# Kernel optimization log

Hardware: AMD Instinct MI355X
Metric: run time of the kernel (lower is better)

## Reference

```python
import jax, jax.numpy as jnp
import numpy as np

C = 128   # desc_dim
NQ = 8
NK = 32768

def setup_inputs() -> dict:
    k = jax.random.key(0)
    ks = jax.random.split(k, 9)
    query = jax.random.normal(ks[0], (1, C, NQ), dtype=jnp.float32)
    keys = jax.random.normal(ks[1], (1, C, NK), dtype=jnp.float32)
    value = jax.random.normal(ks[2], (1, C, NK), dtype=jnp.float32)
    dist = jax.random.normal(ks[3], (1, C, NQ * NK), dtype=jnp.float32)
    mask = jax.random.randint(ks[4], (1, NQ, NK), 0, 2).astype(bool)
    # MLP([3C, C, 1]) as 1x1 Conv1d weights (kernel size 1 -> plain matmuls)
    W1 = jax.random.normal(ks[5], (C, 3 * C), dtype=jnp.float32) * (1.0 / np.sqrt(3 * C))
    b1 = jax.random.normal(ks[6], (C,), dtype=jnp.float32) * 0.01
    W2 = jax.random.normal(ks[7], (1, C), dtype=jnp.float32) * (1.0 / np.sqrt(C))
    b2 = jax.random.normal(ks[8], (1,), dtype=jnp.float32) * 0.01
    return {"query": query, "keys": keys, "value": value, "dist": dist,
            "mask": mask, "W1": W1, "b1": b1, "W2": W2, "b2": b2}

def reference(query, keys, value, dist, mask, W1, b1, W2, b2):
    b = query.shape[0]
    nq, nk = query.shape[-1], keys.shape[-1]
    # pairwise concat: [b, 3C, nq*nk] (faithful to the torch repeat-expand)
    q_e = jnp.broadcast_to(query[:, :, :, None], (b, query.shape[1], nq, nk)).reshape(b, -1, nq * nk)
    k_e = jnp.broadcast_to(keys[:, :, None, :], (b, keys.shape[1], nq, nk)).reshape(b, -1, nq * nk)
    cat = jnp.concatenate([q_e, k_e, dist], axis=1)            # [b, 3C, nq*nk]
    h = jax.nn.relu(jnp.einsum('oc,bcl->bol', W1, cat) + b1[None, :, None])
    s = jnp.einsum('oc,bcl->bol', W2, h) + b2[None, :, None]   # [b, 1, nq*nk]
    scores = s.reshape(b, nq, nk)
    # mask branch (bool tensor): push masked-out entries below the min
    floor = jax.lax.stop_gradient(scores.min()) - 20.0
    scores = scores + floor * (~mask).astype(scores.dtype).reshape(1, nq, nk)
    prob = jax.nn.softmax(scores, axis=-1)                     # [b, nq, nk]
    out = jnp.einsum('bnm,bdm->bdn', prob, value)              # [b, C, nq]
    return out, scores
```

## Files before the change

### kernel.cpp

```cpp
#include <hip/hip_runtime.h>
#include <hip/hip_bf16.h>
#include <math.h>

#define C_    128
#define NQ_   8
#define NK_   32768
#define QNK_  (NQ_*NK_)
#define KT_   32
#define NBLK_ (NK_/KT_)
#define NCH_  256

#define AQ_OFF     0
#define MINKEY_OFF 1024
#define DENOM_OFF  1040
#define OUTV_OFF   4096
#define WSA_OFF    266240

typedef float f32x4 __attribute__((ext_vector_type(4)));
typedef int   i32x4 __attribute__((ext_vector_type(4)));
typedef short bf16x8 __attribute__((ext_vector_type(8)));

__device__ inline unsigned short f2bf(float f){
  unsigned u = __float_as_uint(f);
  return (unsigned short)((u + 0x7FFFu + ((u >> 16) & 1u)) >> 16);
}
__device__ inline unsigned int pkbf(float a, float b){
  __hip_bfloat162 h = __float22bfloat162_rn(make_float2(a, b));
  union { __hip_bfloat162 h2; unsigned int u; } cv; cv.h2 = h; return cv.u;
}
__device__ inline unsigned int fkey(float f){
  unsigned u = __float_as_uint(f);
  return (u & 0x80000000u) ? ~u : (u | 0x80000000u);
}
__device__ inline float fkey_dec(unsigned key){
  unsigned u = (key & 0x80000000u) ? (key & 0x7FFFFFFFu) : ~key;
  return __uint_as_float(u);
}
__device__ inline int swz8(int r){ return ((r ^ (r >> 3)) & 7) << 3; }

__global__ __launch_bounds__(256) void prep_kernel(const float* __restrict__ query,
    const float* __restrict__ W1, const float* __restrict__ b1, float* __restrict__ ws){
  const int t = threadIdx.x;
  if (t == 0) *(unsigned int*)(ws + MINKEY_OFF) = 0xFFFFFFFFu;
  unsigned int* wsa = (unsigned int*)(ws + WSA_OFF);
  for (int u = t; u < 16384; u += 256){
    unsigned int pack = 0;
#pragma unroll
    for (int e2 = 0; e2 < 2; e2++){
      const int E = u*2 + e2;
      const int f = E >> 9, lane = (E >> 3) & 63, e = E & 7;
      const int w = f >> 4, r = f & 15;
      const int part = r >> 3, ks = (r >> 1) & 3, of = r & 1;
      const int o = w*32 + of*16 + (lane & 15);
      const int c = ks*32 + ((lane >> 4) << 3) + e;
      pack |= (unsigned int)f2bf(W1[o*384 + 128 + part*128 + c]) << (16*e2);
    }
    wsa[u] = pack;
  }
  if (t < 128){
    const int o = t;
    float s[8];
#pragma unroll
    for (int q = 0; q < 8; q++) s[q] = b1[o];
    for (int c = 0; c < 128; c++){
      const float wv = W1[o*384 + c];
#pragma unroll
      for (int q = 0; q < 8; q++) s[q] += wv * query[c*8 + q];
    }
#pragma unroll
    for (int q = 0; q < 8; q++) ws[AQ_OFF + q*128 + o] = s[q];
  }
}

template<bool NT>
__device__ inline void stage_load(const float* __restrict__ src, size_t rstride,
                                  int scp, int skl4, f32x4* ra, f32x4* rb){
#pragma unroll
  for (int i = 0; i < 2; i++){
    const float* pa = src + (size_t)(2*scp + 64*i)*rstride + skl4;
    const float* pb = pa + rstride;
    if (NT){ ra[i] = __builtin_nontemporal_load((const f32x4*)pa);
             rb[i] = __builtin_nontemporal_load((const f32x4*)pb); }
    else   { ra[i] = *(const f32x4*)pa; rb[i] = *(const f32x4*)pb; }
  }
}
__device__ inline void stage_write(unsigned short* __restrict__ lds,
                                   int scp, int skl4, const f32x4* ra, const f32x4* rb){
#pragma unroll
  for (int i = 0; i < 2; i++){
    const int c = 2*scp + 64*i;
#pragma unroll
    for (int j = 0; j < 4; j++){
      const int kl = skl4 + j;
      const int idx = (kl*128 + c) ^ swz8(kl);
      *(unsigned int*)&lds[idx] = pkbf(ra[i][j], rb[i][j]);
    }
  }
}
__device__ inline bf16x8 frag_read(const unsigned short* __restrict__ lds,
                                   int cf, int ks, int g, int li){
  const int row = (cf << 4) + li;
  const int idx = (row << 7) + (((ks << 5) + (g << 3)) ^ swz8(row));
  return *(const bf16x8*)&lds[idx];
}

__global__ __launch_bounds__(256, 3) void scores_kernel(
    const float* __restrict__ keys, const float* __restrict__ dist,
    const float* __restrict__ W2, const float* __restrict__ b2p,
    float* __restrict__ ws, float* __restrict__ scores)
{
  __shared__ unsigned short k_lds[KT_*128];
  __shared__ unsigned short d_lds[2][KT_*128];
  __shared__ float aq_lds[NQ_*128];
  __shared__ float red[4][KT_];

  const int t = threadIdx.x, w = t >> 6, l = t & 63;
  const int g = l >> 4, li = l & 15;
  const int blk = blockIdx.x, k0 = blk * KT_;
  const int o0 = w * 32;

  const bf16x8* wsa8 = (const bf16x8*)(ws + WSA_OFF);
  bf16x8 afr[16];
#pragma unroll
  for (int f = 0; f < 16; f++) afr[f] = wsa8[(w*16 + f)*64 + l];

  const f32x4 w2v0 = *(const f32x4*)&W2[o0 + (g<<2)];
  const f32x4 w2v1 = *(const f32x4*)&W2[o0 + 16 + (g<<2)];
  const float b2v = b2p[0];

  for (int i = t; i < NQ_*128; i += 256) aq_lds[i] = ws[AQ_OFF + i];

  const int skl4 = (t & 7) * 4;
  const int scp  = t >> 3;

  f32x4 ra[2], rb[2], ka[2], kb[2];
  stage_load<false>(keys + k0, NK_, scp, skl4, ka, kb);
  stage_load<true >(dist + k0, QNK_, scp, skl4, ra, rb);
  stage_write(k_lds, scp, skl4, ka, kb);
  __syncthreads();

  f32x4 bk[2][2];
#pragma unroll
  for (int cf = 0; cf < 2; cf++)
#pragma unroll
    for (int of = 0; of < 2; of++){ f32x4 z = {0.f,0.f,0.f,0.f}; bk[cf][of] = z; }
#pragma unroll
  for (int ks = 0; ks < 4; ks++){
#pragma unroll
    for (int cf = 0; cf < 2; cf++){
      const bf16x8 b = frag_read(k_lds, cf, ks, g, li);
      bk[cf][0] = __builtin_amdgcn_mfma_f32_16x16x32_bf16(afr[ks*2+0], b, bk[cf][0], 0,0,0);
      bk[cf][1] = __builtin_amdgcn_mfma_f32_16x16x32_bf16(afr[ks*2+1], b, bk[cf][1], 0,0,0);
    }
  }

  stage_write(d_lds[0], scp, skl4, ra, rb);
  stage_load<true>(dist + NK_ + k0, QNK_, scp, skl4, ra, rb);
  __syncthreads();

  float minv = INFINITY;

  for (int q = 0; q < NQ_; q++){
    const unsigned short* db = d_lds[q & 1];
    f32x4 acc[2][2];
#pragma unroll
    for (int cf = 0; cf < 2; cf++)
#pragma unroll
      for (int of = 0; of < 2; of++) acc[cf][of] = bk[cf][of];

#pragma unroll
    for (int ks = 0; ks < 4; ks++){
#pragma unroll
      for (int cf = 0; cf < 2; cf++){
        const bf16x8 b = frag_read(db, cf, ks, g, li);
        acc[cf][0] = __builtin_amdgcn_mfma_f32_16x16x32_bf16(afr[8+ks*2+0], b, acc[cf][0], 0,0,0);
        acc[cf][1] = __builtin_amdgcn_mfma_f32_16x16x32_bf16(afr[8+ks*2+1], b, acc[cf][1], 0,0,0);
      }
    }

    const f32x4 aqv0 = *(const f32x4*)&aq_lds[q*128 + o0 + (g<<2)];
    const f32x4 aqv1 = *(const f32x4*)&aq_lds[q*128 + o0 + 16 + (g<<2)];
#pragma unroll
    for (int cf = 0; cf < 2; cf++){
      float s = 0.f;
#pragma unroll
      for (int r = 0; r < 4; r++){
        s += w2v0[r] * fmaxf(acc[cf][0][r] + aqv0[r], 0.f);
        s += w2v1[r] * fmaxf(acc[cf][1][r] + aqv1[r], 0.f);
      }
      s += __shfl_xor(s, 16, 64);
      s += __shfl_xor(s, 32, 64);
      if (l < 16) red[w][(cf<<4) + l] = s;
    }
    __syncthreads();

    if (q < 7){
      stage_write(d_lds[(q+1)&1], scp, skl4, ra, rb);
      if (q < 6) stage_load<true>(dist + (size_t)(q+2)*NK_ + k0, QNK_, scp, skl4, ra, rb);
    }
    if (t < 32){
      float s = b2v + red[0][t] + red[1][t] + red[2][t] + red[3][t];
      scores[(size_t)q*NK_ + k0 + t] = s;
      minv = fminf(minv, s);
    }
    __syncthreads();
  }

  if (t < 32){
#pragma unroll
    for (int off = 16; off > 0; off >>= 1) minv = fminf(minv, __shfl_xor(minv, off, 64));
    if (t == 0) atomicMin((unsigned int*)(ws + MINKEY_OFF), fkey(minv));
  }
}

__global__ __launch_bounds__(256) void softmax_pv_kernel(
    const float* __restrict__ value, const int* __restrict__ mask,
    float* __restrict__ scores, float* __restrict__ ws)
{
  __shared__ float v_lds[128*128];
  __shared__ __align__(16) float e_lds[8][128];
  __shared__ float wsum[8];
  const int t = threadIdx.x, bid = blockIdx.x, k0 = bid*128;
  const float floorv = fkey_dec(*(const unsigned int*)(ws + MINKEY_OFF)) - 20.0f;

  for (int i = t; i < 4096; i += 256){
    const int d = i >> 5, k4 = (i & 31)*4;
    const f32x4 v = __builtin_nontemporal_load((const f32x4*)&value[(size_t)d*NK_ + k0 + k4]);
    const int dw = (d*128 + k4) ^ ((d & 31) << 2);
    *(f32x4*)&v_lds[dw] = v;
  }

  {
    const int q = t >> 5, kk = (t & 31)*4;
    const size_t gi = (size_t)q*NK_ + k0 + kk;
    const f32x4 s4 = *(const f32x4*)&scores[gi];
    const i32x4 m4 = *(const i32x4*)&mask[gi];
    f32x4 sf, e;
#pragma unroll
    for (int j = 0; j < 4; j++){
      sf[j] = m4[j] ? s4[j] : s4[j] + floorv;
      e[j]  = __expf(sf[j]);
    }
    *(f32x4*)&scores[gi] = sf;
    *(f32x4*)&e_lds[q][kk] = e;
    float es = e[0] + e[1] + e[2] + e[3];
#pragma unroll
    for (int off = 16; off > 0; off >>= 1) es += __shfl_xor(es, off, 64);
    if ((t & 31) == 0) wsum[q] = es;
  }
  __syncthreads();
  if (t < 8) ws[DENOM_OFF + t*NCH_ + bid] = wsum[t];

  const int d = t & 127, qb = (t >> 7)*4;
  f32x4 acc = {0.f,0.f,0.f,0.f};
#pragma unroll 8
  for (int k4 = 0; k4 < 128; k4 += 4){
    const int dw = (d*128 + k4) ^ ((d & 31) << 2);
    const f32x4 v  = *(const f32x4*)&v_lds[dw];
    const f32x4 e0 = *(const f32x4*)&e_lds[qb+0][k4];
    const f32x4 e1 = *(const f32x4*)&e_lds[qb+1][k4];
    const f32x4 e2 = *(const f32x4*)&e_lds[qb+2][k4];
    const f32x4 e3 = *(const f32x4*)&e_lds[qb+3][k4];
#pragma unroll
    for (int j = 0; j < 4; j++){
      acc[0] += v[j]*e0[j]; acc[1] += v[j]*e1[j];
      acc[2] += v[j]*e2[j]; acc[3] += v[j]*e3[j];
    }
  }
#pragma unroll
  for (int j = 0; j < 4; j++) ws[OUTV_OFF + (size_t)bid*1024 + d*8 + qb + j] = acc[j];
}

__global__ __launch_bounds__(256) void finalize_kernel(const float* __restrict__ ws,
    float* __restrict__ out){
  __shared__ float dsum[8];
  __shared__ float red[8][32];
  const int t = threadIdx.x, bid = blockIdx.x;

  if (t < 64){
    const int q = t >> 3, i = t & 7;
    float s = 0.f;
    for (int j = 0; j < 32; j++) s += ws[DENOM_OFF + q*NCH_ + i + 8*j];
#pragma unroll
    for (int off = 4; off > 0; off >>= 1) s += __shfl_xor(s, off, 64);
    if (i == 0) dsum[q] = s;
  }

  const int ol = t & 31, part = t >> 5;
  float s = 0.f;
  for (int j = 0; j < 32; j++)
    s += ws[OUTV_OFF + (size_t)(part + 8*j)*1024 + bid*32 + ol];
  red[part][ol] = s;
  __syncthreads();

  if (t < 32){
    float a = 0.f;
#pragma unroll
    for (int p = 0; p < 8; p++) a += red[p][t];
    const int o = bid*32 + t;
    out[o] = a / dsum[o & 7];
  }
}

extern "C" void kernel_launch(void* const* d_in, const int* in_sizes, int n_in,
                              void* d_out, int out_size, void* d_ws, size_t ws_size,
                              hipStream_t stream){
  const float* query=(const float*)d_in[0];
  const float* keys =(const float*)d_in[1];
  const float* value=(const float*)d_in[2];
  const float* dist =(const float*)d_in[3];
  const int*   mask =(const int*)d_in[4];
  const float* W1   =(const float*)d_in[5];
  const float* b1   =(const float*)d_in[6];
  const float* W2   =(const float*)d_in[7];
  const float* b2   =(const float*)d_in[8];
  float* out=(float*)d_out;
  float* scores=out+1024;
  float* ws=(float*)d_ws;

  prep_kernel      <<<1,256,0,stream>>>(query,W1,b1,ws);
  scores_kernel    <<<NBLK_,256,0,stream>>>(keys,dist,W2,b2,ws,scores);
  softmax_pv_kernel<<<NCH_,256,0,stream>>>(value,mask,scores,ws);
  finalize_kernel  <<<32,256,0,stream>>>(ws,out);
}
```

Baseline: 67.19 us.

## Triple-buffer dist tiles, defer score reduction, and parallelize weight prep

```diff
diff --git a/kernel.cpp b/kernel.cpp
--- a/kernel.cpp
+++ b/kernel.cpp
@@ -40,35 +40,38 @@
 
 __global__ __launch_bounds__(256) void prep_kernel(const float* __restrict__ query,
     const float* __restrict__ W1, const float* __restrict__ b1, float* __restrict__ ws){
-  const int t = threadIdx.x;
-  if (t == 0) *(unsigned int*)(ws + MINKEY_OFF) = 0xFFFFFFFFu;
-  unsigned int* wsa = (unsigned int*)(ws + WSA_OFF);
-  for (int u = t; u < 16384; u += 256){
-    unsigned int pack = 0;
-#pragma unroll
-    for (int e2 = 0; e2 < 2; e2++){
-      const int E = u*2 + e2;
-      const int f = E >> 9, lane = (E >> 3) & 63, e = E & 7;
-      const int w = f >> 4, r = f & 15;
-      const int part = r >> 3, ks = (r >> 1) & 3, of = r & 1;
-      const int o = w*32 + of*16 + (lane & 15);
-      const int c = ks*32 + ((lane >> 4) << 3) + e;
-      pack |= (unsigned int)f2bf(W1[o*384 + 128 + part*128 + c]) << (16*e2);
-    }
-    wsa[u] = pack;
-  }
-  if (t < 128){
-    const int o = t;
-    float s[8];
-#pragma unroll
-    for (int q = 0; q < 8; q++) s[q] = b1[o];
-    for (int c = 0; c < 128; c++){
-      const float wv = W1[o*384 + c];
-#pragma unroll
-      for (int q = 0; q < 8; q++) s[q] += wv * query[c*8 + q];
-    }
-#pragma unroll
-    for (int q = 0; q < 8; q++) ws[AQ_OFF + q*128 + o] = s[q];
+  const int t = threadIdx.x, b = blockIdx.x;
+  if (b < 16){
+    unsigned int* wsa = (unsigned int*)(ws + WSA_OFF);
+    for (int u = b*1024 + t; u < (b+1)*1024; u += 256){
+      unsigned int pack = 0;
+#pragma unroll
+      for (int e2 = 0; e2 < 2; e2++){
+        const int E = u*2 + e2;
+        const int f = E >> 9, lane = (E >> 3) & 63, e = E & 7;
+        const int w = f >> 4, r = f & 15;
+        const int part = r >> 3, ks = (r >> 1) & 3, of = r & 1;
+        const int o = w*32 + of*16 + (lane & 15);
+        const int c = ks*32 + ((lane >> 4) << 3) + e;
+        pack |= (unsigned int)f2bf(W1[o*384 + 128 + part*128 + c]) << (16*e2);
+      }
+      wsa[u] = pack;
+    }
+  } else {
+    if (t == 0) *(unsigned int*)(ws + MINKEY_OFF) = 0xFFFFFFFFu;
+    if (t < 128){
+      const int o = t;
+      float s[8];
+#pragma unroll
+      for (int q = 0; q < 8; q++) s[q] = b1[o];
+      for (int c = 0; c < 128; c++){
+        const float wv = W1[o*384 + c];
+#pragma unroll
+        for (int q = 0; q < 8; q++) s[q] += wv * query[c*8 + q];
+      }
+#pragma unroll
+      for (int q = 0; q < 8; q++) ws[AQ_OFF + q*128 + o] = s[q];
+    }
   }
 }
 
@@ -110,9 +113,9 @@
     float* __restrict__ ws, float* __restrict__ scores)
 {
   __shared__ unsigned short k_lds[KT_*128];
-  __shared__ unsigned short d_lds[2][KT_*128];
+  __shared__ unsigned short d_lds[3][KT_*128];
   __shared__ float aq_lds[NQ_*128];
-  __shared__ float red[4][KT_];
+  __shared__ float red[4][256];
 
   const int t = threadIdx.x, w = t >> 6, l = t & 63;
   const int g = l >> 4, li = l & 15;
@@ -120,9 +123,9 @@
   const int o0 = w * 32;
 
   const bf16x8* wsa8 = (const bf16x8*)(ws + WSA_OFF);
-  bf16x8 afr[16];
-#pragma unroll
-  for (int f = 0; f < 16; f++) afr[f] = wsa8[(w*16 + f)*64 + l];
+  bf16x8 afr_d[8];
+#pragma unroll
+  for (int f = 0; f < 8; f++) afr_d[f] = wsa8[(w*16 + 8 + f)*64 + l];
 
   const f32x4 w2v0 = *(const f32x4*)&W2[o0 + (g<<2)];
   const f32x4 w2v1 = *(const f32x4*)&W2[o0 + 16 + (g<<2)];
@@ -133,10 +136,14 @@
   const int skl4 = (t & 7) * 4;
   const int scp  = t >> 3;
 
-  f32x4 ra[2], rb[2], ka[2], kb[2];
+  f32x4 ka[2], kb[2], a0[2], b0[2], a1[2], b1[2], ra[2], rb[2];
   stage_load<false>(keys + k0, NK_, scp, skl4, ka, kb);
-  stage_load<true >(dist + k0, QNK_, scp, skl4, ra, rb);
-  stage_write(k_lds, scp, skl4, ka, kb);
+  stage_load<true >(dist + k0,             QNK_, scp, skl4, a0, b0);
+  stage_load<true >(dist + (size_t)1*NK_ + k0, QNK_, scp, skl4, a1, b1);
+  stage_load<true >(dist + (size_t)2*NK_ + k0, QNK_, scp, skl4, ra, rb);
+  stage_write(k_lds,    scp, skl4, ka, kb);
+  stage_write(d_lds[0], scp, skl4, a0, b0);
+  stage_write(d_lds[1], scp, skl4, a1, b1);
   __syncthreads();
 
   f32x4 bk[2][2];
@@ -144,37 +151,40 @@
   for (int cf = 0; cf < 2; cf++)
 #pragma unroll
     for (int of = 0; of < 2; of++){ f32x4 z = {0.f,0.f,0.f,0.f}; bk[cf][of] = z; }
-#pragma unroll
-  for (int ks = 0; ks < 4; ks++){
-#pragma unroll
-    for (int cf = 0; cf < 2; cf++){
-      const bf16x8 b = frag_read(k_lds, cf, ks, g, li);
-      bk[cf][0] = __builtin_amdgcn_mfma_f32_16x16x32_bf16(afr[ks*2+0], b, bk[cf][0], 0,0,0);
-      bk[cf][1] = __builtin_amdgcn_mfma_f32_16x16x32_bf16(afr[ks*2+1], b, bk[cf][1], 0,0,0);
-    }
-  }
-
-  stage_write(d_lds[0], scp, skl4, ra, rb);
-  stage_load<true>(dist + NK_ + k0, QNK_, scp, skl4, ra, rb);
-  __syncthreads();
-
-  float minv = INFINITY;
-
+  {
+    bf16x8 afk[8];
+#pragma unroll
+    for (int f = 0; f < 8; f++) afk[f] = wsa8[(w*16 + f)*64 + l];
+#pragma unroll
+    for (int ks = 0; ks < 4; ks++){
+#pragma unroll
+      for (int cf = 0; cf < 2; cf++){
+        const bf16x8 b = frag_read(k_lds, cf, ks, g, li);
+        bk[cf][0] = __builtin_amdgcn_mfma_f32_16x16x32_bf16(afk[ks*2+0], b, bk[cf][0], 0,0,0);
+        bk[cf][1] = __builtin_amdgcn_mfma_f32_16x16x32_bf16(afk[ks*2+1], b, bk[cf][1], 0,0,0);
+      }
+    }
+  }
+
+  float ps[8][2];
+#pragma unroll
   for (int q = 0; q < NQ_; q++){
-    const unsigned short* db = d_lds[q & 1];
+    if (q <= 5) stage_write(d_lds[(q+2)%3], scp, skl4, ra, rb);
+    if (q <= 4) stage_load<true>(dist + (size_t)(q+3)*NK_ + k0, QNK_, scp, skl4, ra, rb);
+
+    const unsigned short* db = d_lds[q % 3];
     f32x4 acc[2][2];
 #pragma unroll
     for (int cf = 0; cf < 2; cf++)
 #pragma unroll
       for (int of = 0; of < 2; of++) acc[cf][of] = bk[cf][of];
-
 #pragma unroll
     for (int ks = 0; ks < 4; ks++){
 #pragma unroll
       for (int cf = 0; cf < 2; cf++){
         const bf16x8 b = frag_read(db, cf, ks, g, li);
-        acc[cf][0] = __builtin_amdgcn_mfma_f32_16x16x32_bf16(afr[8+ks*2+0], b, acc[cf][0], 0,0,0);
-        acc[cf][1] = __builtin_amdgcn_mfma_f32_16x16x32_bf16(afr[8+ks*2+1], b, acc[cf][1], 0,0,0);
+        acc[cf][0] = __builtin_amdgcn_mfma_f32_16x16x32_bf16(afr_d[ks*2+0], b, acc[cf][0], 0,0,0);
+        acc[cf][1] = __builtin_amdgcn_mfma_f32_16x16x32_bf16(afr_d[ks*2+1], b, acc[cf][1], 0,0,0);
       }
     }
 
@@ -190,26 +200,28 @@
       }
       s += __shfl_xor(s, 16, 64);
       s += __shfl_xor(s, 32, 64);
-      if (l < 16) red[w][(cf<<4) + l] = s;
+      ps[q][cf] = s;
     }
     __syncthreads();
-
-    if (q < 7){
-      stage_write(d_lds[(q+1)&1], scp, skl4, ra, rb);
-      if (q < 6) stage_load<true>(dist + (size_t)(q+2)*NK_ + k0, QNK_, scp, skl4, ra, rb);
-    }
-    if (t < 32){
-      float s = b2v + red[0][t] + red[1][t] + red[2][t] + red[3][t];
-      scores[(size_t)q*NK_ + k0 + t] = s;
-      minv = fminf(minv, s);
-    }
-    __syncthreads();
-  }
-
-  if (t < 32){
-#pragma unroll
-    for (int off = 16; off > 0; off >>= 1) minv = fminf(minv, __shfl_xor(minv, off, 64));
-    if (t == 0) atomicMin((unsigned int*)(ws + MINKEY_OFF), fkey(minv));
+  }
+
+  if (g == 0){
+#pragma unroll
+    for (int q = 0; q < NQ_; q++){
+      red[w][q*32 + li]      = ps[q][0];
+      red[w][q*32 + 16 + li] = ps[q][1];
+    }
+  }
+  __syncthreads();
+
+  {
+    const int q = t >> 5, col = t & 31;
+    const float s = b2v + red[0][t] + red[1][t] + red[2][t] + red[3][t];
+    __builtin_nontemporal_store(s, &scores[(size_t)q*NK_ + k0 + col]);
+    float m = s;
+#pragma unroll
+    for (int off = 32; off > 0; off >>= 1) m = fminf(m, __shfl_xor(m, off, 64));
+    if (l == 0) atomicMin((unsigned int*)(ws + MINKEY_OFF), fkey(m));
   }
 }
 
@@ -241,7 +253,7 @@
       sf[j] = m4[j] ? s4[j] : s4[j] + floorv;
       e[j]  = __expf(sf[j]);
     }
-    *(f32x4*)&scores[gi] = sf;
+    __builtin_nontemporal_store(sf, (f32x4*)&scores[gi]);
     *(f32x4*)&e_lds[q][kk] = e;
     float es = e[0] + e[1] + e[2] + e[3];
 #pragma unroll
@@ -318,7 +330,7 @@
   float* scores=out+1024;
   float* ws=(float*)d_ws;
 
-  prep_kernel      <<<1,256,0,stream>>>(query,W1,b1,ws);
+  prep_kernel      <<<17,256,0,stream>>>(query,W1,b1,ws);
   scores_kernel    <<<NBLK_,256,0,stream>>>(keys,dist,W2,b2,ws,scores);
   softmax_pv_kernel<<<NCH_,256,0,stream>>>(value,mask,scores,ws);
   finalize_kernel  <<<32,256,0,stream>>>(ws,out);
```

New measurement: 93.83 us. 1.4x slower.

## Restructure scores kernel to per-wave key tiles with LDS-shared W1 fragments

Applied to the files above, without the earlier changes.

```diff
diff --git a/kernel.cpp b/kernel.cpp
--- a/kernel.cpp
+++ b/kernel.cpp
@@ -6,8 +6,9 @@
 #define NQ_   8
 #define NK_   32768
 #define QNK_  (NQ_*NK_)
-#define KT_   32
-#define NBLK_ (NK_/KT_)
+#define KW_   16
+#define KTB_  64
+#define NSB_  512
 #define NCH_  256
 
 #define AQ_OFF     0
@@ -40,176 +41,181 @@
 
 __global__ __launch_bounds__(256) void prep_kernel(const float* __restrict__ query,
     const float* __restrict__ W1, const float* __restrict__ b1, float* __restrict__ ws){
-  const int t = threadIdx.x;
-  if (t == 0) *(unsigned int*)(ws + MINKEY_OFF) = 0xFFFFFFFFu;
-  unsigned int* wsa = (unsigned int*)(ws + WSA_OFF);
-  for (int u = t; u < 16384; u += 256){
-    unsigned int pack = 0;
-#pragma unroll
-    for (int e2 = 0; e2 < 2; e2++){
-      const int E = u*2 + e2;
-      const int f = E >> 9, lane = (E >> 3) & 63, e = E & 7;
-      const int w = f >> 4, r = f & 15;
-      const int part = r >> 3, ks = (r >> 1) & 3, of = r & 1;
-      const int o = w*32 + of*16 + (lane & 15);
-      const int c = ks*32 + ((lane >> 4) << 3) + e;
-      pack |= (unsigned int)f2bf(W1[o*384 + 128 + part*128 + c]) << (16*e2);
-    }
-    wsa[u] = pack;
-  }
-  if (t < 128){
-    const int o = t;
-    float s[8];
-#pragma unroll
-    for (int q = 0; q < 8; q++) s[q] = b1[o];
-    for (int c = 0; c < 128; c++){
-      const float wv = W1[o*384 + c];
-#pragma unroll
-      for (int q = 0; q < 8; q++) s[q] += wv * query[c*8 + q];
-    }
-#pragma unroll
-    for (int q = 0; q < 8; q++) ws[AQ_OFF + q*128 + o] = s[q];
-  }
-}
-
-template<bool NT>
-__device__ inline void stage_load(const float* __restrict__ src, size_t rstride,
-                                  int scp, int skl4, f32x4* ra, f32x4* rb){
-#pragma unroll
-  for (int i = 0; i < 2; i++){
-    const float* pa = src + (size_t)(2*scp + 64*i)*rstride + skl4;
-    const float* pb = pa + rstride;
-    if (NT){ ra[i] = __builtin_nontemporal_load((const f32x4*)pa);
-             rb[i] = __builtin_nontemporal_load((const f32x4*)pb); }
-    else   { ra[i] = *(const f32x4*)pa; rb[i] = *(const f32x4*)pb; }
-  }
-}
-__device__ inline void stage_write(unsigned short* __restrict__ lds,
-                                   int scp, int skl4, const f32x4* ra, const f32x4* rb){
-#pragma unroll
-  for (int i = 0; i < 2; i++){
-    const int c = 2*scp + 64*i;
+  const int t = threadIdx.x, b = blockIdx.x;
+  if (b < 16){
+    unsigned int* wsa = (unsigned int*)(ws + WSA_OFF);
+    for (int u = b*1024 + t; u < (b+1)*1024; u += 256){
+      unsigned int pack = 0;
+#pragma unroll
+      for (int e2 = 0; e2 < 2; e2++){
+        const int E = u*2 + e2;
+        const int f = E >> 9, lane = (E >> 3) & 63, e = E & 7;
+        const int w = f >> 4, r = f & 15;
+        const int part = r >> 3, ks = (r >> 1) & 3, of = r & 1;
+        const int o = w*32 + of*16 + (lane & 15);
+        const int c = ks*32 + ((lane >> 4) << 3) + e;
+        pack |= (unsigned int)f2bf(W1[o*384 + 128 + part*128 + c]) << (16*e2);
+      }
+      wsa[u] = pack;
+    }
+  } else {
+    if (t == 0) *(unsigned int*)(ws + MINKEY_OFF) = 0xFFFFFFFFu;
+    if (t < 128){
+      const int o = t;
+      float s[8];
+#pragma unroll
+      for (int q = 0; q < 8; q++) s[q] = b1[o];
+      for (int c = 0; c < 128; c++){
+        const float wv = W1[o*384 + c];
+#pragma unroll
+        for (int q = 0; q < 8; q++) s[q] += wv * query[c*8 + q];
+      }
+#pragma unroll
+      for (int q = 0; q < 8; q++) ws[AQ_OFF + q*128 + o] = s[q];
+    }
+  }
+}
+
+__device__ inline void stage16_load(const float* __restrict__ src, size_t rstride,
+                                    int l, f32x4* ra, f32x4* rb){
+  const int skl = (l & 3) * 4;
+  const int c2  = (l >> 2) * 2;
+#pragma unroll
+  for (int p = 0; p < 4; p++){
+    const float* pa = src + (size_t)(p*32 + c2)*rstride + skl;
+    ra[p] = __builtin_nontemporal_load((const f32x4*)pa);
+    rb[p] = __builtin_nontemporal_load((const f32x4*)(pa + rstride));
+  }
+}
+__device__ inline void stage16_write(unsigned short* __restrict__ lds,
+                                     int l, const f32x4* ra, const f32x4* rb){
+  const int skl = (l & 3) * 4;
+  const int c2  = (l >> 2) * 2;
+#pragma unroll
+  for (int p = 0; p < 4; p++){
+    const int c = p*32 + c2;
 #pragma unroll
     for (int j = 0; j < 4; j++){
-      const int kl = skl4 + j;
+      const int kl = skl + j;
       const int idx = (kl*128 + c) ^ swz8(kl);
-      *(unsigned int*)&lds[idx] = pkbf(ra[i][j], rb[i][j]);
-    }
-  }
-}
-__device__ inline bf16x8 frag_read(const unsigned short* __restrict__ lds,
-                                   int cf, int ks, int g, int li){
-  const int row = (cf << 4) + li;
-  const int idx = (row << 7) + (((ks << 5) + (g << 3)) ^ swz8(row));
+      *(unsigned int*)&lds[idx] = pkbf(ra[p][j], rb[p][j]);
+    }
+  }
+}
+__device__ inline bf16x8 frag16_read(const unsigned short* __restrict__ lds,
+                                     int ks, int g, int li){
+  const int idx = (li << 7) + (((ks << 5) + (g << 3)) ^ swz8(li));
   return *(const bf16x8*)&lds[idx];
 }
 
-__global__ __launch_bounds__(256, 3) void scores_kernel(
+__global__ __launch_bounds__(256, 2) void scores_kernel(
     const float* __restrict__ keys, const float* __restrict__ dist,
     const float* __restrict__ W2, const float* __restrict__ b2p,
     float* __restrict__ ws, float* __restrict__ scores)
 {
-  __shared__ unsigned short k_lds[KT_*128];
-  __shared__ unsigned short d_lds[2][KT_*128];
+  __shared__ unsigned short a_lds[32*512];
+  __shared__ unsigned short d_lds[4][KW_*128];
   __shared__ float aq_lds[NQ_*128];
-  __shared__ float red[4][KT_];
+  __shared__ float w2_lds[128];
+  __shared__ float minred[4];
 
   const int t = threadIdx.x, w = t >> 6, l = t & 63;
   const int g = l >> 4, li = l & 15;
-  const int blk = blockIdx.x, k0 = blk * KT_;
-  const int o0 = w * 32;
-
-  const bf16x8* wsa8 = (const bf16x8*)(ws + WSA_OFF);
-  bf16x8 afr[16];
-#pragma unroll
-  for (int f = 0; f < 16; f++) afr[f] = wsa8[(w*16 + f)*64 + l];
-
-  const f32x4 w2v0 = *(const f32x4*)&W2[o0 + (g<<2)];
-  const f32x4 w2v1 = *(const f32x4*)&W2[o0 + 16 + (g<<2)];
+  const int blk = blockIdx.x;
+  const int k0w = blk*KTB_ + w*KW_;
+  unsigned short* dw = d_lds[w];
+
+  const unsigned int* wsaU = (const unsigned int*)(ws + WSA_OFF);
+  unsigned int* aU = (unsigned int*)a_lds;
+  for (int i = t; i < 8192; i += 256){
+    const int s = i >> 8, r = i & 255;
+    aU[i] = wsaU[((s >> 3)*16 + (s & 7))*256 + r];
+  }
+  for (int i = t; i < NQ_*128; i += 256) aq_lds[i] = ws[AQ_OFF + i];
+  if (t < 128) w2_lds[t] = W2[t];
+
+  f32x4 rA[4], rB[4], rC[4], rD[4];
+  stage16_load(keys + k0w, NK_, l, rA, rB);
+  stage16_write(dw, l, rA, rB);
+  stage16_load(dist + k0w, QNK_, l, rA, rB);
+  __syncthreads();
+
+  f32x4 bk[8];
+#pragma unroll
+  for (int f = 0; f < 8; f++){ f32x4 z = {0.f,0.f,0.f,0.f}; bk[f] = z; }
+#pragma unroll
+  for (int ks = 0; ks < 4; ks++){
+    const bf16x8 bfr = frag16_read(dw, ks, g, li);
+#pragma unroll
+    for (int of8 = 0; of8 < 8; of8++){
+      const int s = (of8 >> 1)*8 + ks*2 + (of8 & 1);
+      const bf16x8 a = *(const bf16x8*)&a_lds[s*512 + l*8];
+      bk[of8] = __builtin_amdgcn_mfma_f32_16x16x32_bf16(a, bfr, bk[of8], 0,0,0);
+    }
+  }
+  __syncthreads();
+
+  for (int i = t; i < 8192; i += 256){
+    const int s = i >> 8, r = i & 255;
+    aU[i] = wsaU[((s >> 3)*16 + 8 + (s & 7))*256 + r];
+  }
+  __syncthreads();
+
   const float b2v = b2p[0];
-
-  for (int i = t; i < NQ_*128; i += 256) aq_lds[i] = ws[AQ_OFF + i];
-
-  const int skl4 = (t & 7) * 4;
-  const int scp  = t >> 3;
-
-  f32x4 ra[2], rb[2], ka[2], kb[2];
-  stage_load<false>(keys + k0, NK_, scp, skl4, ka, kb);
-  stage_load<true >(dist + k0, QNK_, scp, skl4, ra, rb);
-  stage_write(k_lds, scp, skl4, ka, kb);
-  __syncthreads();
-
-  f32x4 bk[2][2];
-#pragma unroll
-  for (int cf = 0; cf < 2; cf++)
-#pragma unroll
-    for (int of = 0; of < 2; of++){ f32x4 z = {0.f,0.f,0.f,0.f}; bk[cf][of] = z; }
-#pragma unroll
-  for (int ks = 0; ks < 4; ks++){
-#pragma unroll
-    for (int cf = 0; cf < 2; cf++){
-      const bf16x8 b = frag_read(k_lds, cf, ks, g, li);
-      bk[cf][0] = __builtin_amdgcn_mfma_f32_16x16x32_bf16(afr[ks*2+0], b, bk[cf][0], 0,0,0);
-      bk[cf][1] = __builtin_amdgcn_mfma_f32_16x16x32_bf16(afr[ks*2+1], b, bk[cf][1], 0,0,0);
-    }
-  }
-
-  stage_write(d_lds[0], scp, skl4, ra, rb);
-  stage_load<true>(dist + NK_ + k0, QNK_, scp, skl4, ra, rb);
-  __syncthreads();
-
   float minv = INFINITY;
 
-  for (int q = 0; q < NQ_; q++){
-    const unsigned short* db = d_lds[q & 1];
-    f32x4 acc[2][2];
-#pragma unroll
-    for (int cf = 0; cf < 2; cf++)
-#pragma unroll
-      for (int of = 0; of < 2; of++) acc[cf][of] = bk[cf][of];
-
-#pragma unroll
-    for (int ks = 0; ks < 4; ks++){
-#pragma unroll
-      for (int cf = 0; cf < 2; cf++){
-        const bf16x8 b = frag_read(db, cf, ks, g, li);
-        acc[cf][0] = __builtin_amdgcn_mfma_f32_16x16x32_bf16(afr[8+ks*2+0], b, acc[cf][0], 0,0,0);
-        acc[cf][1] = __builtin_amdgcn_mfma_f32_16x16x32_bf16(afr[8+ks*2+1], b, acc[cf][1], 0,0,0);
-      }
-    }
-
-    const f32x4 aqv0 = *(const f32x4*)&aq_lds[q*128 + o0 + (g<<2)];
-    const f32x4 aqv1 = *(const f32x4*)&aq_lds[q*128 + o0 + 16 + (g<<2)];
-#pragma unroll
-    for (int cf = 0; cf < 2; cf++){
-      float s = 0.f;
-#pragma unroll
-      for (int r = 0; r < 4; r++){
-        s += w2v0[r] * fmaxf(acc[cf][0][r] + aqv0[r], 0.f);
-        s += w2v1[r] * fmaxf(acc[cf][1][r] + aqv1[r], 0.f);
-      }
-      s += __shfl_xor(s, 16, 64);
-      s += __shfl_xor(s, 32, 64);
-      if (l < 16) red[w][(cf<<4) + l] = s;
-    }
-    __syncthreads();
-
-    if (q < 7){
-      stage_write(d_lds[(q+1)&1], scp, skl4, ra, rb);
-      if (q < 6) stage_load<true>(dist + (size_t)(q+2)*NK_ + k0, QNK_, scp, skl4, ra, rb);
-    }
-    if (t < 32){
-      float s = b2v + red[0][t] + red[1][t] + red[2][t] + red[3][t];
-      scores[(size_t)q*NK_ + k0 + t] = s;
-      minv = fminf(minv, s);
-    }
-    __syncthreads();
-  }
-
-  if (t < 32){
-#pragma unroll
-    for (int off = 16; off > 0; off >>= 1) minv = fminf(minv, __shfl_xor(minv, off, 64));
-    if (t == 0) atomicMin((unsigned int*)(ws + MINKEY_OFF), fkey(minv));
+#define SCORE_ITER(Q, RA, RB, RA2, RB2)                                          \
+  {                                                                              \
+    if ((Q) < 7) stage16_load(dist + (size_t)((Q)+1)*NK_ + k0w, QNK_, l, RA2, RB2); \
+    stage16_write(dw, l, RA, RB);                                                \
+    f32x4 acc[8];                                                                \
+    _Pragma("unroll")                                                            \
+    for (int f = 0; f < 8; f++) acc[f] = bk[f];                                  \
+    _Pragma("unroll")                                                            \
+    for (int ks = 0; ks < 4; ks++){                                              \
+      const bf16x8 bfr = frag16_read(dw, ks, g, li);                             \
+      _Pragma("unroll")                                                          \
+      for (int of8 = 0; of8 < 8; of8++){                                         \
+        const int s = (of8 >> 1)*8 + ks*2 + (of8 & 1);                           \
+        const bf16x8 a = *(const bf16x8*)&a_lds[s*512 + l*8];                    \
+        acc[of8] = __builtin_amdgcn_mfma_f32_16x16x32_bf16(a, bfr, acc[of8], 0,0,0); \
+      }                                                                          \
+    }                                                                            \
+    float sv = 0.f;                                                              \
+    _Pragma("unroll")                                                            \
+    for (int of8 = 0; of8 < 8; of8++){                                           \
+      const int ob = (of8 >> 1)*32 + (of8 & 1)*16 + g*4;                         \
+      const f32x4 aqv = *(const f32x4*)&aq_lds[(Q)*128 + ob];                    \
+      const f32x4 w2v = *(const f32x4*)&w2_lds[ob];                              \
+      _Pragma("unroll")                                                          \
+      for (int r = 0; r < 4; r++)                                                \
+        sv += w2v[r] * fmaxf(acc[of8][r] + aqv[r], 0.f);                         \
+    }                                                                            \
+    sv += __shfl_xor(sv, 16, 64);                                                \
+    sv += __shfl_xor(sv, 32, 64);                                                \
+    sv += b2v;                                                                   \
+    if (l < 16)                                                                  \
+      __builtin_nontemporal_store(sv, &scores[(size_t)(Q)*NK_ + k0w + l]);       \
+    minv = fminf(minv, sv);                                                      \
+  }
+
+  SCORE_ITER(0, rA, rB, rC, rD)
+  SCORE_ITER(1, rC, rD, rA, rB)
+  SCORE_ITER(2, rA, rB, rC, rD)
+  SCORE_ITER(3, rC, rD, rA, rB)
+  SCORE_ITER(4, rA, rB, rC, rD)
+  SCORE_ITER(5, rC, rD, rA, rB)
+  SCORE_ITER(6, rA, rB, rC, rD)
+  SCORE_ITER(7, rC, rD, rA, rB)
+#undef SCORE_ITER
+
+#pragma unroll
+  for (int off = 32; off > 0; off >>= 1) minv = fminf(minv, __shfl_xor(minv, off, 64));
+  if (l == 0) minred[w] = minv;
+  __syncthreads();
+  if (t == 0){
+    const float m = fminf(fminf(minred[0], minred[1]), fminf(minred[2], minred[3]));
+    atomicMin((unsigned int*)(ws + MINKEY_OFF), fkey(m));
   }
 }
 
@@ -241,7 +247,7 @@
       sf[j] = m4[j] ? s4[j] : s4[j] + floorv;
       e[j]  = __expf(sf[j]);
     }
-    *(f32x4*)&scores[gi] = sf;
+    __builtin_nontemporal_store(sf, (f32x4*)&scores[gi]);
     *(f32x4*)&e_lds[q][kk] = e;
     float es = e[0] + e[1] + e[2] + e[3];
 #pragma unroll
@@ -318,8 +324,8 @@
   float* scores=out+1024;
   float* ws=(float*)d_ws;
 
-  prep_kernel      <<<1,256,0,stream>>>(query,W1,b1,ws);
-  scores_kernel    <<<NBLK_,256,0,stream>>>(keys,dist,W2,b2,ws,scores);
+  prep_kernel      <<<17,256,0,stream>>>(query,W1,b1,ws);
+  scores_kernel    <<<NSB_,256,0,stream>>>(keys,dist,W2,b2,ws,scores);
   softmax_pv_kernel<<<NCH_,256,0,stream>>>(value,mask,scores,ws);
   finalize_kernel  <<<32,256,0,stream>>>(ws,out);
 }
```

New measurement: 65.69 us. 2.2% less time.
